# Optimization experiments

Measured on AMD Instinct MI355X. Metric: run time of the kernel, lower is better.

Reference implementation:

```python
import jax, jax.numpy as jnp
import numpy as np

B, T, C, H, N_LAYER, LAYER_ID = 4, 2048, 1024, 16, 12, 6
N = C // H
Q = 256  # T % 256 == 0 -> chunk size used by the module


def setup_inputs():
    key = jax.random.key(0)
    ks = jax.random.split(key, 9)
    r0 = LAYER_ID / (N_LAYER - 1)
    r1 = 1.0 - LAYER_ID / N_LAYER
    ddd = (jnp.arange(C, dtype=jnp.float32) / C)[None, None, :]
    h = jnp.arange(C, dtype=jnp.float32)
    s = 1.0 / np.sqrt(C)
    return {
        "x": jax.random.normal(ks[0], (B, T, C), jnp.float32),
        "time_maa_x": 1.0 - ddd ** r1,
        "time_maa_w": 1.0 - ddd ** r1,
        "time_maa_k": 1.0 - ddd ** r1,
        "time_maa_v": 1.0 - (ddd ** r1 + 0.3 * r0),
        "time_maa_r": 1.0 - ddd ** (0.5 * r1),
        "maa_w1": jax.random.uniform(ks[1], (C, 4 * 32), jnp.float32, minval=-0.01, maxval=0.01),
        "maa_w2": jax.random.uniform(ks[2], (4, 32, C), jnp.float32, minval=-0.01, maxval=0.01),
        "decay_w1": jax.random.uniform(ks[3], (C, 64), jnp.float32, minval=-0.01, maxval=0.01),
        "decay_w2": jax.random.uniform(ks[4], (64, C), jnp.float32, minval=-0.01, maxval=0.01),
        "time_decay": (-6.0 + 5.0 * (h / (C - 1)) ** (0.7 + 1.3 * r0))[None, None, :],
        "time_faaaa": (r0 * (1.0 - h / (C - 1))).reshape(1, H, 1, 1, N),
        "Wr": jax.random.normal(ks[5], (C, C), jnp.float32) * s,
        "Wk": jax.random.normal(ks[6], (C, C), jnp.float32) * s,
        "Wv": jax.random.normal(ks[7], (C, C), jnp.float32) * s,
        "Wo": jax.random.normal(ks[8], (C, C), jnp.float32) * s,
        "ln_g": jnp.ones((C,), jnp.float32),
        "ln_b": jnp.zeros((C,), jnp.float32),
    }


def _forward(x, time_maa_x, time_maa_w, time_maa_k, time_maa_v, time_maa_r,
             maa_w1, maa_w2, decay_w1, decay_w2, time_decay, time_faaaa,
             Wr, Wk, Wv, Wo, ln_g, ln_b):
    b, t, c = x.shape
    nc = t // Q
    # time_shift: zero-pad one step at front of time axis, drop last step
    xx = jnp.pad(x, ((0, 0), (1, 0), (0, 0)))[:, :-1] - x
    xxx = x + xx * time_maa_x
    m = jnp.tanh(xxx @ maa_w1).reshape(b, t, 4, -1)  # [B,T,4,32]
    m = jnp.einsum('btfd,fdc->fbtc', m, maa_w2)       # [4,B,T,C]
    mw, mk, mv, mr = m[0], m[1], m[2], m[3]
    xw = x + xx * (time_maa_w + mw)
    xk = x + xx * (time_maa_k + mk)
    xv = x + xx * (time_maa_v + mv)
    xr = x + xx * (time_maa_r + mr)
    r = (xr @ Wr).reshape(b, t, H, N).transpose(0, 2, 1, 3)  # [B,H,T,N]
    k = (xk @ Wk).reshape(b, t, H, N).transpose(0, 2, 1, 3)
    v = (xv @ Wv).reshape(b, t, H, N).transpose(0, 2, 1, 3)
    w = time_decay + jnp.tanh(xw @ decay_w1) @ decay_w2      # [B,T,C]
    w = w.reshape(b, t, H, N).transpose(0, 2, 1, 3).mean(axis=-1)  # [B,H,T]
    w_log = -jnp.exp(w)
    wc = w_log.reshape(b, H, nc, Q, 1)
    wc_cum = jnp.cumsum(wc, axis=-2)
    shifted = jnp.pad(wc_cum, ((0, 0), (0, 0), (0, 0), (1, 0), (0, 0)))[..., :-1, :]
    ws_log = wc.sum(axis=-2, keepdims=True)   # [B,H,nc,1,1]
    w_inter = jnp.exp(ws_log - wc_cum)        # [B,H,nc,Q,1]
    w_intra = jnp.exp(wc_cum - wc)            # [B,H,nc,Q,1]
    ws = jnp.exp(ws_log)                      # [B,H,nc,1,1]
    A = shifted - jnp.swapaxes(wc_cum, -1, -2)  # [B,H,nc,Q,Q]
    strict = jnp.tril(jnp.ones((Q, Q), dtype=bool), -1)
    # torch: tril() -> exp() -> tril(-1)  ==  exp on strict-lower, zero elsewhere
    w_mask = jnp.where(strict, jnp.exp(jnp.where(strict, A, 0.0)), 0.0)
    rr = r.reshape(b, H, nc, Q, N)
    kk = k.reshape(b, H, nc, Q, N)
    vv = v.reshape(b, H, nc, Q, N)
    kv = jnp.einsum('bhcqn,bhcqm->bhcnm', kk * w_inter, vv)  # [B,H,nc,N,N]

    def step(state, inp):
        ws_i, kv_i = inp
        return ws_i * state + kv_i, state  # emit state BEFORE update (as in torch loop)

    _, states = jax.lax.scan(step, jnp.zeros((b, H, N, N), x.dtype),
                             (jnp.moveaxis(ws, 2, 0), jnp.moveaxis(kv, 2, 0)))
    states = jnp.moveaxis(states, 0, 2)  # [B,H,nc,N,N]
    inter = jnp.einsum('bhcqn,bhcnm->bhcqm', rr * w_intra, states)
    scores = jnp.einsum('bhcqn,bhckn->bhcqk', rr, kk) * w_mask
    diag = jnp.sum(rr * (time_faaaa * kk), axis=-1)  # [B,H,nc,Q]
    intra = jnp.einsum('bhcqk,bhckm->bhcqm', scores, vv) + diag[..., None] * vv
    y = (inter + intra).reshape(b, H, t, N).transpose(0, 2, 1, 3).reshape(b, t, c)
    mu = y.mean(axis=-1, keepdims=True)
    var = ((y - mu) ** 2).mean(axis=-1, keepdims=True)
    y = (y - mu) / jnp.sqrt(var + 1e-5) * ln_g + ln_b  # ln_x
    return y @ Wo  # output projection (dropout p=0)


def reference(x, time_maa_x, time_maa_w, time_maa_k, time_maa_v, time_maa_r,
              maa_w1, maa_w2, decay_w1, decay_w2, time_decay, time_faaaa,
              Wr, Wk, Wv, Wo, ln_g, ln_b):
    return _forward(x, time_maa_x, time_maa_w, time_maa_k, time_maa_v, time_maa_r,
                    maa_w1, maa_w2, decay_w1, decay_w2, time_decay, time_faaaa,
                    Wr, Wk, Wv, Wo, ln_g, ln_b)
```

## Files before the change

kernel.cpp:

```cpp
#include <hip/hip_runtime.h>
#include <math.h>

#define BB 4
#define TT 2048
#define CC 1024
#define HH 16
#define NN 64
#define QQ 256
#define NCH 8
#define BT 8192

typedef unsigned short u16;
typedef __attribute__((ext_vector_type(8))) short bf16x8;
typedef __attribute__((ext_vector_type(4))) short bf16x4;
typedef __attribute__((ext_vector_type(4))) float f32x4;
typedef __attribute__((ext_vector_type(4))) u16 u16x4;

__device__ inline u16 f2b(float x) {
  union { float f; unsigned u; } v;
  v.f = x;
  unsigned r = v.u + 0x7FFFu + ((v.u >> 16) & 1u);
  return (u16)(r >> 16);
}
__device__ inline float b2f(u16 u) {
  union { unsigned u; float f; } v;
  v.u = ((unsigned)u) << 16;
  return v.f;
}
__device__ inline bf16x8 ldfrag(const u16* p) {
  bf16x4 lo = *(const bf16x4*)p;
  bf16x4 hi = *(const bf16x4*)(p + 4);
  return __builtin_shufflevector(lo, hi, 0, 1, 2, 3, 4, 5, 6, 7);
}
__device__ inline void stage_tile(const u16* __restrict__ g, size_t base,
                                  int pitch, int tid, u16* __restrict__ lds) {
#pragma unroll
  for (int it = 0; it < 2; it++) {
    int cidx = tid + it * 256;
    int r = cidx >> 3, c8 = (cidx & 7) * 8;
    bf16x8 v = *(const bf16x8*)(g + base + (size_t)r * pitch + c8);
    *(bf16x4*)(lds + r * 72 + c8) = __builtin_shufflevector(v, v, 0, 1, 2, 3);
    *(bf16x4*)(lds + r * 72 + c8 + 4) = __builtin_shufflevector(v, v, 4, 5, 6, 7);
  }
}

__global__ __launch_bounds__(256) void mix_kernel(const float* __restrict__ x,
                                                  const float* __restrict__ tmx,
                                                  u16* __restrict__ xxxb) {
  size_t e = ((size_t)blockIdx.x * 256 + threadIdx.x) * 4;
  int c = (int)(e & 1023);
  size_t row = e >> 10;
  int t = (int)(row & 2047);
  float4 xv = *(const float4*)(x + e);
  float4 pv = make_float4(0.f, 0.f, 0.f, 0.f);
  if (t > 0) pv = *(const float4*)(x + e - 1024);
  float4 d = make_float4(pv.x - xv.x, pv.y - xv.y, pv.z - xv.z, pv.w - xv.w);
  u16x4 o;
  o.x = f2b(xv.x + d.x * tmx[c + 0]);
  o.y = f2b(xv.y + d.y * tmx[c + 1]);
  o.z = f2b(xv.z + d.z * tmx[c + 2]);
  o.w = f2b(xv.w + d.w * tmx[c + 3]);
  *(u16x4*)(xxxb + e) = o;
}

__global__ __launch_bounds__(256) void cvt_wT(const float* __restrict__ W0,
                                              const float* __restrict__ W1,
                                              const float* __restrict__ W2,
                                              const float* __restrict__ W3,
                                              u16* __restrict__ O0,
                                              u16* __restrict__ O1,
                                              u16* __restrict__ O2,
                                              u16* __restrict__ O3) {
  const float* W;
  u16* O;
  switch (blockIdx.z) {
    case 0: W = W0; O = O0; break;
    case 1: W = W1; O = O1; break;
    case 2: W = W2; O = O2; break;
    default: W = W3; O = O3; break;
  }
  __shared__ float t[64][65];
  int bx = blockIdx.x * 64;
  int by = blockIdx.y * 64;
#pragma unroll
  for (int it = 0; it < 16; it++) {
    int idx = it * 256 + threadIdx.x;
    int r = idx >> 6, c = idx & 63;
    t[r][c] = W[(size_t)(by + r) * 1024 + bx + c];
  }
  __syncthreads();
#pragma unroll
  for (int it = 0; it < 16; it++) {
    int idx = it * 256 + threadIdx.x;
    int n = idx >> 6, k = idx & 63;
    O[(size_t)(bx + n) * 1024 + by + k] = f2b(t[k][n]);
  }
}

__global__ __launch_bounds__(256) void cvt3_T(const float* __restrict__ w1,
                                              const float* __restrict__ w2,
                                              const float* __restrict__ d1,
                                              u16* __restrict__ o1,
                                              u16* __restrict__ o2,
                                              u16* __restrict__ o3) {
  const float* in;
  u16* out;
  int R, C;
  switch (blockIdx.z) {
    case 0: in = w1; out = o1; R = 1024; C = 128; break;
    case 1: in = w2; out = o2; R = 128; C = 1024; break;
    default: in = d1; out = o3; R = 1024; C = 64; break;
  }
  int c0 = blockIdx.x * 64, r0 = blockIdx.y * 64;
  if (c0 >= C || r0 >= R) return;
  __shared__ float t[64][65];
#pragma unroll
  for (int it = 0; it < 16; it++) {
    int idx = it * 256 + threadIdx.x;
    int r = idx >> 6, c = idx & 63;
    t[r][c] = in[(size_t)(r0 + r) * C + c0 + c];
  }
  __syncthreads();
#pragma unroll
  for (int it = 0; it < 16; it++) {
    int idx = it * 256 + threadIdx.x;
    int c = idx >> 6, r = idx & 63;
    out[(size_t)(c0 + c) * R + r0 + r] = f2b(t[r][c]);
  }
}

__global__ __launch_bounds__(256) void gemm_maa(const u16* __restrict__ A,
                                                const u16* __restrict__ Bt,
                                                u16* __restrict__ Cb) {
  __shared__ u16 As[64 * 32];
  __shared__ u16 Bs[128 * 32];
  const int tid = threadIdx.x;
  const int lane = tid & 63;
  const int wave = tid >> 6;
  const int wc = wave * 32;
  const int fr = lane & 15;
  const int fq = lane >> 4;
  const int row0 = blockIdx.x * 64;

  f32x4 acc[4][2];
#pragma unroll
  for (int i = 0; i < 4; i++)
#pragma unroll
    for (int j = 0; j < 2; j++) acc[i][j] = (f32x4){0.f, 0.f, 0.f, 0.f};

  const int ra = tid >> 2, ca = (tid & 3) * 8;
  const int rb1 = ra + 64;

  for (int k0 = 0; k0 < 1024; k0 += 32) {
    __builtin_amdgcn_global_load_lds(
        (const __attribute__((address_space(1))) void*)(A + (size_t)(row0 + ra) * 1024 + k0 + ca),
        (__attribute__((address_space(3))) void*)(As + tid * 8), 16, 0, 0);
    __builtin_amdgcn_global_load_lds(
        (const __attribute__((address_space(1))) void*)(Bt + (size_t)ra * 1024 + k0 + ca),
        (__attribute__((address_space(3))) void*)(Bs + tid * 8), 16, 0, 0);
    __builtin_amdgcn_global_load_lds(
        (const __attribute__((address_space(1))) void*)(Bt + (size_t)rb1 * 1024 + k0 + ca),
        (__attribute__((address_space(3))) void*)(Bs + (tid + 256) * 8), 16, 0, 0);
    __syncthreads();
    bf16x8 af[4], bf[2];
#pragma unroll
    for (int i = 0; i < 4; i++)
      af[i] = *(const bf16x8*)(As + ((i * 16 + fr) * 32 + fq * 8));
#pragma unroll
    for (int j = 0; j < 2; j++)
      bf[j] = *(const bf16x8*)(Bs + ((wc + j * 16 + fr) * 32 + fq * 8));
#pragma unroll
    for (int i = 0; i < 4; i++)
#pragma unroll
      for (int j = 0; j < 2; j++)
        acc[i][j] = __builtin_amdgcn_mfma_f32_16x16x32_bf16(af[i], bf[j], acc[i][j], 0, 0, 0);
    __syncthreads();
  }
#pragma unroll
  for (int i = 0; i < 4; i++) {
    int grow = row0 + i * 16 + fq * 4;
#pragma unroll
    for (int j = 0; j < 2; j++) {
      int gcol = wc + j * 16 + fr;
#pragma unroll
      for (int r = 0; r < 4; r++)
        Cb[(size_t)(grow + r) * 128 + gcol] = f2b(tanhf(acc[i][j][r]));
    }
  }
}

#define DP_ABUF 8192
#define DP_BBUF 16384
#define DP_SBUF 24576
#define DP_SMEM_BYTES 147456

template <bool TRIPLE, bool F32OUT>
__global__ __launch_bounds__(512, 2) void gemm_dp(
    const u16* __restrict__ A0, const u16* __restrict__ A1,
    const u16* __restrict__ A2, const u16* __restrict__ B0,
    const u16* __restrict__ B1, const u16* __restrict__ B2,
    float* __restrict__ Cf, u16* __restrict__ C0, u16* __restrict__ C1,
    u16* __restrict__ C2) {
  extern __shared__ __align__(16) u16 smem[];
  const int nwg = (int)(gridDim.x * gridDim.y * gridDim.z);
  const int wg = (int)(blockIdx.x + (blockIdx.y << 2) + (blockIdx.z << 8));
  const int cpx = nwg >> 3;
  const int swz = (wg & 7) * cpx + (wg >> 3);
  const int bx = swz & 3;
  const int by = (swz >> 2) & 63;
  const int bz = swz >> 8;

  const u16* __restrict__ A;
  const u16* __restrict__ Bt;
  u16* __restrict__ Cb;
  if (TRIPLE) {
    switch (bz) {
      case 0: A = A0; Bt = B0; Cb = C0; break;
      case 1: A = A1; Bt = B1; Cb = C1; break;
      default: A = A2; Bt = B2; Cb = C2; break;
    }
  } else {
    A = A0; Bt = B0; Cb = C0;
  }

  const int tid = threadIdx.x;
  const int lane = tid & 63;
  const int wave = tid >> 6;
  const int wr = (wave >> 2) * 64;
  const int wc = (wave & 3) * 64;
  const int fr = lane & 15;
  const int fq = lane >> 4;
  const int s8 = fr & 7;
  const int row0 = by * 128;
  const int col0 = bx * 256;

  int aoff[4][2], boff[4][2];
#pragma unroll
  for (int mi = 0; mi < 4; mi++)
#pragma unroll
    for (int ks = 0; ks < 2; ks++)
      aoff[mi][ks] = (wr + mi * 16 + fr) * 64 + (((ks * 4 + fq) ^ s8) * 8);
#pragma unroll
  for (int nj = 0; nj < 4; nj++)
#pragma unroll
    for (int ks = 0; ks < 2; ks++)
      boff[nj][ks] = (wc + nj * 16 + fr) * 64 + (((ks * 4 + fq) ^ s8) * 8);

  auto stage = [&](int kt, int q) {
    const u16* __restrict__ gA = A + (size_t)row0 * 1024 + kt * 64;
    const u16* __restrict__ gB = Bt + (size_t)col0 * 1024 + kt * 64;
    u16* dA = smem + q * DP_SBUF;
    u16* dB = dA + DP_ABUF;
#pragma unroll
    for (int p = 0; p < 2; p++) {
      int pos = tid + p * 512;
      int r = pos >> 3, gch = (pos & 7) ^ (r & 7);
      __builtin_amdgcn_global_load_lds(
          (const __attribute__((address_space(1))) void*)(gA + (size_t)r * 1024 + gch * 8),
          (__attribute__((address_space(3))) void*)(dA + pos * 8), 16, 0, 0);
    }
#pragma unroll
    for (int p = 0; p < 4; p++) {
      int pos = tid + p * 512;
      int r = pos >> 3, gch = (pos & 7) ^ (r & 7);
      __builtin_amdgcn_global_load_lds(
          (const __attribute__((address_space(1))) void*)(gB + (size_t)r * 1024 + gch * 8),
          (__attribute__((address_space(3))) void*)(dB + pos * 8), 16, 0, 0);
    }
  };

  f32x4 acc[4][4];
#pragma unroll
  for (int mi = 0; mi < 4; mi++)
#pragma unroll
    for (int nj = 0; nj < 4; nj++) acc[mi][nj] = (f32x4){0.f, 0.f, 0.f, 0.f};

  auto iter_body = [&](int qc, int qs, bool dostage, int t2) {
    if (dostage) stage(t2, qs);
    const u16* sA = smem + qc * DP_SBUF;
    const u16* sB = sA + DP_ABUF;
    bf16x8 av[4][2], bv[4][2];
#pragma unroll
    for (int mi = 0; mi < 4; mi++)
#pragma unroll
      for (int ks = 0; ks < 2; ks++)
        av[mi][ks] = *(const bf16x8*)(sA + aoff[mi][ks]);
#pragma unroll
    for (int nj = 0; nj < 4; nj++)
#pragma unroll
      for (int ks = 0; ks < 2; ks++)
        bv[nj][ks] = *(const bf16x8*)(sB + boff[nj][ks]);
    __builtin_amdgcn_s_setprio(1);
#pragma unroll
    for (int ks = 0; ks < 2; ks++)
#pragma unroll
      for (int mi = 0; mi < 4; mi++)
#pragma unroll
        for (int nj = 0; nj < 4; nj++)
          acc[mi][nj] = __builtin_amdgcn_mfma_f32_16x16x32_bf16(
              av[mi][ks], bv[nj][ks], acc[mi][nj], 0, 0, 0);
    __builtin_amdgcn_s_setprio(0);
  };

  stage(0, 0);
  stage(1, 1);
  int qc = 0, qs = 2;
  for (int t = 0; t < 14; t++) {
    asm volatile("s_waitcnt vmcnt(6)" ::: "memory");
    __builtin_amdgcn_s_barrier();
    iter_body(qc, qs, true, t + 2);
    qc = (qc == 2) ? 0 : qc + 1;
    qs = (qs == 2) ? 0 : qs + 1;
  }
  asm volatile("s_waitcnt vmcnt(6)" ::: "memory");
  __builtin_amdgcn_s_barrier();
  iter_body(qc, 0, false, 0);
  qc = (qc == 2) ? 0 : qc + 1;
  asm volatile("s_waitcnt vmcnt(0)" ::: "memory");
  __builtin_amdgcn_s_barrier();
  iter_body(qc, 0, false, 0);

#pragma unroll
  for (int mi = 0; mi < 4; mi++) {
    int grow = row0 + wr + mi * 16 + fq * 4;
#pragma unroll
    for (int nj = 0; nj < 4; nj++) {
      int gcol = col0 + wc + nj * 16 + fr;
#pragma unroll
      for (int r = 0; r < 4; r++) {
        if (F32OUT)
          Cf[(size_t)(grow + r) * 1024 + gcol] = acc[mi][nj][r];
        else
          Cb[(size_t)(grow + r) * 1024 + gcol] = f2b(acc[mi][nj][r]);
      }
    }
  }
}

__global__ __launch_bounds__(256) void blend_mfma(
    const u16* __restrict__ mb, const u16* __restrict__ w2T,
    const float* __restrict__ x,
    const float* __restrict__ tmw, const float* __restrict__ tmk,
    const float* __restrict__ tmv, const float* __restrict__ tmr,
    u16* __restrict__ xwb, u16* __restrict__ xkb, u16* __restrict__ xvb,
    u16* __restrict__ xrb) {
  __shared__ u16 mS[64 * 136];
  __shared__ u16 wS[64 * 136];
  const int tid = threadIdx.x;
  const int lane = tid & 63;
  const int w = tid >> 6;
  const int fr = lane & 15;
  const int fq = lane >> 4;
  const int c0 = blockIdx.x * 64;
  const int bt0 = blockIdx.y * 64;

#pragma unroll
  for (int it = 0; it < 4; it++) {
    int idx = tid + it * 256;
    int r = idx >> 4, c8 = (idx & 15) * 8;
    bf16x8 v = *(const bf16x8*)(mb + (size_t)(bt0 + r) * 128 + c8);
    *(bf16x4*)(mS + r * 136 + c8) = __builtin_shufflevector(v, v, 0, 1, 2, 3);
    *(bf16x4*)(mS + r * 136 + c8 + 4) = __builtin_shufflevector(v, v, 4, 5, 6, 7);
    bf16x8 u = *(const bf16x8*)(w2T + (size_t)(c0 + r) * 128 + c8);
    *(bf16x4*)(wS + r * 136 + c8) = __builtin_shufflevector(u, u, 0, 1, 2, 3);
    *(bf16x4*)(wS + r * 136 + c8 + 4) = __builtin_shufflevector(u, u, 4, 5, 6, 7);
  }
  __syncthreads();

  f32x4 acc[4][4];
#pragma unroll
  for (int j = 0; j < 4; j++)
#pragma unroll
    for (int f = 0; f < 4; f++) acc[j][f] = (f32x4){0.f, 0.f, 0.f, 0.f};

#pragma unroll
  for (int f = 0; f < 4; f++) {
    bf16x8 aA = ldfrag(mS + (w * 16 + fr) * 136 + f * 32 + fq * 8);
#pragma unroll
    for (int j = 0; j < 4; j++) {
      bf16x8 bB = ldfrag(wS + (j * 16 + fr) * 136 + f * 32 + fq * 8);
      acc[j][f] = __builtin_amdgcn_mfma_f32_16x16x32_bf16(aA, bB, acc[j][f], 0, 0, 0);
    }
  }

#pragma unroll
  for (int j = 0; j < 4; j++) {
    int c = c0 + j * 16 + fr;
    float w_ = tmw[c], k_ = tmk[c], v_ = tmv[c], r_ = tmr[c];
#pragma unroll
    for (int rr = 0; rr < 4; rr++) {
      int bt = bt0 + w * 16 + fq * 4 + rr;
      size_t g = (size_t)bt * 1024 + c;
      float xv_ = x[g];
      float xp = ((bt & 2047) != 0) ? x[g - 1024] : 0.f;
      float dx = xp - xv_;
      xwb[g] = f2b(xv_ + dx * (w_ + acc[j][0][rr]));
      xkb[g] = f2b(xv_ + dx * (k_ + acc[j][1][rr]));
      xvb[g] = f2b(xv_ + dx * (v_ + acc[j][2][rr]));
      xrb[g] = f2b(xv_ + dx * (r_ + acc[j][3][rr]));
    }
  }
}

__global__ __launch_bounds__(256) void dw2r_kernel(const float* __restrict__ dw2,
                                                   const float* __restrict__ td,
                                                   float* __restrict__ dw2r,
                                                   float* __restrict__ tdr,
                                                   u16* __restrict__ dw2rbT) {
  int idx = blockIdx.x * 256 + threadIdx.x;
  if (idx < 1024) {
    int j = idx >> 4, h = idx & 15;
    float s = 0.f;
    for (int n = 0; n < 64; n++) s += dw2[(size_t)j * 1024 + h * 64 + n];
    float m = s * (1.f / 64.f);
    dw2r[j * 16 + h] = m;
    dw2rbT[h * 64 + j] = f2b(m);
  }
  if (idx < 16) {
    float s = 0.f;
    for (int n = 0; n < 64; n++) s += td[idx * 64 + n];
    tdr[idx] = s * (1.f / 64.f);
  }
}

__global__ __launch_bounds__(256) void decay_mfma(const u16* __restrict__ xwb,
                                                  const u16* __restrict__ d1T,
                                                  const u16* __restrict__ dw2rbT,
                                                  const float* __restrict__ tdr,
                                                  float* __restrict__ wlog) {
  __shared__ u16 As[64 * 32];
  __shared__ u16 Bs[64 * 32];
  __shared__ u16 h1S[64 * 72];
  __shared__ u16 dwS[16 * 72];
  const int tid = threadIdx.x;
  const int lane = tid & 63;
  const int w = tid >> 6;
  const int fr = lane & 15;
  const int fq = lane >> 4;
  const int bt0 = blockIdx.x * 64;

#pragma unroll
  for (int it = 0; it < 4; it++) {
    int idx = tid + it * 256;
    int r = idx >> 6, c = idx & 63;
    dwS[r * 72 + c] = dw2rbT[r * 64 + c];
  }

  f32x4 acc[4];
#pragma unroll
  for (int j = 0; j < 4; j++) acc[j] = (f32x4){0.f, 0.f, 0.f, 0.f};

  const int ra = tid >> 2, ca = (tid & 3) * 8;
  for (int k0 = 0; k0 < 1024; k0 += 32) {
    __builtin_amdgcn_global_load_lds(
        (const __attribute__((address_space(1))) void*)(xwb + (size_t)(bt0 + ra) * 1024 + k0 + ca),
        (__attribute__((address_space(3))) void*)(As + tid * 8), 16, 0, 0);
    __builtin_amdgcn_global_load_lds(
        (const __attribute__((address_space(1))) void*)(d1T + (size_t)ra * 1024 + k0 + ca),
        (__attribute__((address_space(3))) void*)(Bs + tid * 8), 16, 0, 0);
    __syncthreads();
    bf16x8 aA = *(const bf16x8*)(As + ((w * 16 + fr) * 32 + fq * 8));
#pragma unroll
    for (int j = 0; j < 4; j++) {
      bf16x8 bB = *(const bf16x8*)(Bs + ((j * 16 + fr) * 32 + fq * 8));
      acc[j] = __builtin_amdgcn_mfma_f32_16x16x32_bf16(aA, bB, acc[j], 0, 0, 0);
    }
    __syncthreads();
  }
#pragma unroll
  for (int j = 0; j < 4; j++)
#pragma unroll
    for (int rr = 0; rr < 4; rr++)
      h1S[(w * 16 + fq * 4 + rr) * 72 + j * 16 + fr] = f2b(tanhf(acc[j][rr]));
  __syncthreads();

  f32x4 a2 = (f32x4){0.f, 0.f, 0.f, 0.f};
#pragma unroll
  for (int ks = 0; ks < 2; ks++) {
    bf16x8 aA = ldfrag(h1S + (w * 16 + fr) * 72 + ks * 32 + fq * 8);
    bf16x8 bB = ldfrag(dwS + fr * 72 + ks * 32 + fq * 8);
    a2 = __builtin_amdgcn_mfma_f32_16x16x32_bf16(aA, bB, a2, 0, 0, 0);
  }
  float tdv = tdr[fr];
#pragma unroll
  for (int rr = 0; rr < 4; rr++) {
    int bt = bt0 + w * 16 + fq * 4 + rr;
    int b = bt >> 11, tl = bt & 2047;
    wlog[((size_t)(b * 16 + fr)) * 2048 + tl] = -__expf(tdv + a2[rr]);
  }
}

__global__ __launch_bounds__(256) void wprep_kernel(const float* __restrict__ wlog,
                                                    float* __restrict__ cum,
                                                    float* __restrict__ excl,
                                                    float* __restrict__ wsl) {
  int bid = blockIdx.x;
  int c = bid & 7, bh = bid >> 3;
  int q = threadIdx.x;
  float v = wlog[(size_t)bh * 2048 + c * 256 + q];
  __shared__ float s[256];
  s[q] = v;
  float val = v;
  for (int off = 1; off < 256; off <<= 1) {
    __syncthreads();
    float t = (q >= off) ? s[q - off] : 0.f;
    __syncthreads();
    val += t;
    s[q] = val;
  }
  __syncthreads();
  float total = s[255];
  cum[(size_t)bid * 256 + q] = val;
  excl[(size_t)bid * 256 + q] = val - v;
  if (q == 0) wsl[bid] = total;
}

__global__ __launch_bounds__(256) void kvtrans2_kernel(
    const u16* __restrict__ vb, const u16* __restrict__ kb,
    const u16* __restrict__ rb, const float* __restrict__ faaaa,
    const float* __restrict__ cum, const float* __restrict__ wsl,
    u16* __restrict__ vT, u16* __restrict__ kTw, float* __restrict__ diagG) {
  int tt = blockIdx.x;
  int bh = blockIdx.y;
  int b = bh >> 4, h = bh & 15;
  int cc = tt >> 2;
  int bidc = bh * 8 + cc;
  __shared__ float tv[64][65];
  __shared__ float tk[64][65];
  __shared__ float wfac[64];
  __shared__ float faS[64];
  const int tid = threadIdx.x;
  float wslog = wsl[bidc];
  if (tid < 64) {
    wfac[tid] = __expf(wslog - cum[(size_t)bidc * 256 + (tt & 3) * 64 + tid]);
    faS[tid] = faaaa[h * 64 + tid];
  }
  __syncthreads();
  const int m = tid & 63;
  float fam = faS[m];
#pragma unroll
  for (int it = 0; it < 16; it++) {
    int r = it * 4 + (tid >> 6);
    size_t g = ((size_t)(b * TT + tt * 64 + r)) * CC + h * 64 + m;
    float vraw = b2f(vb[g]);
    float kraw = b2f(kb[g]);
    float rraw = b2f(rb[g]);
    tv[r][m] = vraw;
    tk[r][m] = kraw;
    float s = rraw * fam * kraw;
    s += __shfl_xor(s, 1);
    s += __shfl_xor(s, 2);
    s += __shfl_xor(s, 4);
    s += __shfl_xor(s, 8);
    s += __shfl_xor(s, 16);
    s += __shfl_xor(s, 32);
    if (m == 0) diagG[(size_t)bh * 2048 + tt * 64 + r] = s;
  }
  __syncthreads();
#pragma unroll
  for (int it = 0; it < 16; it++) {
    int idx = it * 256 + tid;
    int mm = idx >> 6, tl = idx & 63;
    size_t o = ((size_t)(bh * 64 + mm)) * TT + tt * 64 + tl;
    vT[o] = f2b(tv[tl][mm]);
    kTw[o] = f2b(tk[tl][mm] * wfac[tl]);
  }
}

__global__ __launch_bounds__(256) void kv_mfma(const u16* __restrict__ kTw,
                                               const u16* __restrict__ vT,
                                               float* __restrict__ kvb) {
  int bid = blockIdx.x;
  int c = bid & 7, bh = bid >> 3;
  __shared__ u16 kS[64 * 72];
  __shared__ u16 vS[64 * 72];
  const int tid = threadIdx.x;
  const int lane = tid & 63;
  const int w = tid >> 6;
  const int fr = lane & 15;
  const int fq = lane >> 4;
  f32x4 acc[4];
#pragma unroll
  for (int j = 0; j < 4; j++) acc[j] = (f32x4){0.f, 0.f, 0.f, 0.f};
  const size_t base = (size_t)bh * 64 * TT + c * QQ;
  for (int qt = 0; qt < 4; qt++) {
    __syncthreads();
    stage_tile(kTw, base + qt * 64, TT, tid, kS);
    stage_tile(vT, base + qt * 64, TT, tid, vS);
    __syncthreads();
#pragma unroll
    for (int ks = 0; ks < 2; ks++) {
      bf16x8 aA = ldfrag(kS + (w * 16 + fr) * 72 + ks * 32 + fq * 8);
#pragma unroll
      for (int j = 0; j < 4; j++) {
        bf16x8 bB = ldfrag(vS + (j * 16 + fr) * 72 + ks * 32 + fq * 8);
        acc[j] = __builtin_amdgcn_mfma_f32_16x16x32_bf16(aA, bB, acc[j], 0, 0, 0);
      }
    }
  }
#pragma unroll
  for (int j = 0; j < 4; j++)
#pragma unroll
    for (int rr = 0; rr < 4; rr++)
      kvb[(size_t)bid * 4096 + (w * 16 + fq * 4 + rr) * 64 + j * 16 + fr] = acc[j][rr];
}

__global__ __launch_bounds__(256) void scan_kernel(const float* __restrict__ kvb,
                                                   const float* __restrict__ wsl,
                                                   float* __restrict__ st) {
  int bh = blockIdx.x >> 2;
  int sl = blockIdx.x & 3;
  int tid = threadIdx.x;
  float s[4];
#pragma unroll
  for (int i = 0; i < 4; i++) s[i] = 0.f;
  for (int c = 0; c < 8; c++) {
    int bid = bh * 8 + c;
    float w = __expf(wsl[bid]);
#pragma unroll
    for (int i = 0; i < 4; i++) {
      size_t e = (size_t)bid * 4096 + sl * 1024 + i * 256 + tid;
      st[e] = s[i];
      s[i] = w * s[i] + kvb[e];
    }
  }
}

__global__ __launch_bounds__(256) void attn_mfma(
    const u16* __restrict__ rb, const u16* __restrict__ kb,
    const u16* __restrict__ vT, const float* __restrict__ stg,
    const float* __restrict__ cum, const float* __restrict__ excl,
    const float* __restrict__ diagG, float* __restrict__ y) {
  int bid = blockIdx.x;
  int c = bid & 7, bh = bid >> 3;
  int b = bh >> 4, h = bh & 15;
  __shared__ u16 rt[64 * 72];
  __shared__ u16 kt[64 * 72];
  __shared__ u16 vt[64 * 72];
  __shared__ u16 pt[64 * 72];
  __shared__ u16 stT[64 * 72];
  __shared__ float cumS[256], exS[256], diagS[256], ekS[256];

  const int tid = threadIdx.x;
  const int lane = tid & 63;
  const int w = tid >> 6;
  const int fr = lane & 15;
  const int fq = lane >> 4;

  cumS[tid] = cum[(size_t)bid * 256 + tid];
  exS[tid] = excl[(size_t)bid * 256 + tid];
  diagS[tid] = diagG[(size_t)bh * 2048 + c * 256 + tid];
#pragma unroll
  for (int it = 0; it < 16; it++) {
    int idx = tid + it * 256;
    int n = idx >> 6, mm = idx & 63;
    stT[mm * 72 + n] = f2b(stg[(size_t)bid * 4096 + idx]);
  }
  __syncthreads();
  const float ccm = cumS[127];
  ekS[tid] = __expf(ccm - cumS[tid]);

  const size_t rowbase = ((size_t)b * TT + c * QQ) * CC + h * 64;
  const size_t vbase0 = (size_t)bh * 64 * TT + c * QQ;

  for (int qt = 0; qt < 4; qt++) {
    __syncthreads();
    stage_tile(rb, rowbase + (size_t)(qt * 64) * CC, CC, tid, rt);
    __syncthreads();

    f32x4 acc[4];
#pragma unroll
    for (int jm = 0; jm < 4; jm++) acc[jm] = (f32x4){0.f, 0.f, 0.f, 0.f};
    bf16x8 rA[2];
    rA[0] = ldfrag(rt + (w * 16 + fr) * 72 + fq * 8);
    rA[1] = ldfrag(rt + (w * 16 + fr) * 72 + 32 + fq * 8);
#pragma unroll
    for (int ks = 0; ks < 2; ks++)
#pragma unroll
      for (int jm = 0; jm < 4; jm++) {
        bf16x8 bB = ldfrag(stT + (jm * 16 + fr) * 72 + ks * 32 + fq * 8);
        acc[jm] = __builtin_amdgcn_mfma_f32_16x16x32_bf16(rA[ks], bB, acc[jm], 0, 0, 0);
      }
    int ql0 = w * 16 + fq * 4;
    float er[4], eqc[4];
#pragma unroll
    for (int rr = 0; rr < 4; rr++) {
      float ex = exS[qt * 64 + ql0 + rr];
      er[rr] = __expf(ex);
      eqc[rr] = __expf(ex - ccm);
    }
#pragma unroll
    for (int jm = 0; jm < 4; jm++)
#pragma unroll
      for (int rr = 0; rr < 4; rr++) acc[jm][rr] *= er[rr];

    for (int kti = 0; kti <= qt; kti++) {
      __syncthreads();
      stage_tile(kb, rowbase + (size_t)(kti * 64) * CC, CC, tid, kt);
      stage_tile(vT, vbase0 + (size_t)(kti * 64), TT, tid, vt);
      __syncthreads();

      f32x4 sacc[4];
#pragma unroll
      for (int jj = 0; jj < 4; jj++) sacc[jj] = (f32x4){0.f, 0.f, 0.f, 0.f};
#pragma unroll
      for (int ks = 0; ks < 2; ks++)
#pragma unroll
        for (int jj = 0; jj < 4; jj++) {
          bf16x8 bB = ldfrag(kt + (jj * 16 + fr) * 72 + ks * 32 + fq * 8);
          sacc[jj] = __builtin_amdgcn_mfma_f32_16x16x32_bf16(rA[ks], bB, sacc[jj], 0, 0, 0);
        }
#pragma unroll
      for (int jj = 0; jj < 4; jj++) {
        int kcol = kti * 64 + jj * 16 + fr;
        float ek = ekS[kcol];
#pragma unroll
        for (int rr = 0; rr < 4; rr++) {
          int qrow = qt * 64 + ql0 + rr;
          float vsc;
          if (kcol < qrow)
            vsc = sacc[jj][rr] * eqc[rr] * ek;
          else if (kcol == qrow)
            vsc = diagS[qrow];
          else
            vsc = 0.f;
          pt[(ql0 + rr) * 72 + jj * 16 + fr] = f2b(vsc);
        }
      }
      __syncthreads();
#pragma unroll
      for (int ks = 0; ks < 2; ks++) {
        bf16x8 pA = ldfrag(pt + (w * 16 + fr) * 72 + ks * 32 + fq * 8);
#pragma unroll
        for (int jm = 0; jm < 4; jm++) {
          bf16x8 vB = ldfrag(vt + (jm * 16 + fr) * 72 + ks * 32 + fq * 8);
          acc[jm] = __builtin_amdgcn_mfma_f32_16x16x32_bf16(pA, vB, acc[jm], 0, 0, 0);
        }
      }
    }
    int qg0 = qt * 64 + w * 16 + fq * 4;
#pragma unroll
    for (int jm = 0; jm < 4; jm++)
#pragma unroll
      for (int rr = 0; rr < 4; rr++)
        y[rowbase + (size_t)(qg0 + rr) * CC + jm * 16 + fr] = acc[jm][rr];
  }
}

__global__ __launch_bounds__(256) void ln_kernel(const float* __restrict__ y,
                                                 const float* __restrict__ g,
                                                 const float* __restrict__ bta,
                                                 u16* __restrict__ out) {
  __shared__ float red[8];
  int bt = blockIdx.x;
  int tid = threadIdx.x;
  float v[4];
  float s = 0.f;
#pragma unroll
  for (int i = 0; i < 4; i++) {
    v[i] = y[(size_t)bt * 1024 + i * 256 + tid];
    s += v[i];
  }
#pragma unroll
  for (int off = 32; off > 0; off >>= 1) s += __shfl_down(s, off);
  if ((tid & 63) == 0) red[tid >> 6] = s;
  __syncthreads();
  if (tid == 0) red[4] = red[0] + red[1] + red[2] + red[3];
  __syncthreads();
  float mu = red[4] * (1.f / 1024.f);
  float s2 = 0.f;
#pragma unroll
  for (int i = 0; i < 4; i++) {
    float d = v[i] - mu;
    s2 += d * d;
  }
#pragma unroll
  for (int off = 32; off > 0; off >>= 1) s2 += __shfl_down(s2, off);
  __syncthreads();
  if ((tid & 63) == 0) red[tid >> 6] = s2;
  __syncthreads();
  if (tid == 0) red[5] = red[0] + red[1] + red[2] + red[3];
  __syncthreads();
  float var = red[5] * (1.f / 1024.f);
  float rstd = rsqrtf(var + 1e-5f);
#pragma unroll
  for (int i = 0; i < 4; i++) {
    int c = i * 256 + tid;
    out[(size_t)bt * 1024 + c] = f2b((v[i] - mu) * rstd * g[c] + bta[c]);
  }
}

extern "C" void kernel_launch(void* const* d_in, const int* in_sizes, int n_in,
                              void* d_out, int out_size, void* d_ws,
                              size_t ws_size, hipStream_t stream) {
  const float* x = (const float*)d_in[0];
  const float* tmx = (const float*)d_in[1];
  const float* tmw = (const float*)d_in[2];
  const float* tmk = (const float*)d_in[3];
  const float* tmv = (const float*)d_in[4];
  const float* tmr = (const float*)d_in[5];
  const float* maa_w1 = (const float*)d_in[6];
  const float* maa_w2 = (const float*)d_in[7];
  const float* decay_w1 = (const float*)d_in[8];
  const float* decay_w2 = (const float*)d_in[9];
  const float* time_decay = (const float*)d_in[10];
  const float* faaaa = (const float*)d_in[11];
  const float* Wr = (const float*)d_in[12];
  const float* Wk = (const float*)d_in[13];
  const float* Wv = (const float*)d_in[14];
  const float* Wo = (const float*)d_in[15];
  const float* lng = (const float*)d_in[16];
  const float* lnb = (const float*)d_in[17];
  float* out = (float*)d_out;
  float* ws = (float*)d_ws;

  const size_t S = (size_t)BT * CC;

  float* y_ = ws;
  float* dw2r = ws + S;
  float* tdr = dw2r + 1024;
  float* wlog = tdr + 1024;
  float* cum = wlog + 131072;
  float* excl = cum + 131072;
  float* wsl = excl + 131072;
  float* diagG = wsl + 1024;
  float* kvb = diagG + 131072;
  float* stb = kvb + (size_t)512 * 4096;
  float* fend = stb + (size_t)512 * 4096;
  u16* xxxb = (u16*)fend;
  u16* mb = xxxb + S;
  u16* xkb = mb + (size_t)BT * 128;
  u16* xvb = xkb + S;
  u16* xrb = xvb + S;
  u16* xwb = xrb + S;
  u16* rb16 = xwb + S;
  u16* kb16 = rb16 + S;
  u16* Vb = kb16 + S;
  u16* Wrt = Vb + S;
  u16* Wkt = Wrt + (size_t)1024 * 1024;
  u16* Wvt = Wkt + (size_t)1024 * 1024;
  u16* Wot = Wvt + (size_t)1024 * 1024;
  u16* w1T = Wot + (size_t)1024 * 1024;
  u16* w2T = w1T + (size_t)128 * 1024;
  u16* d1T = w2T + (size_t)1024 * 128;
  u16* dw2rbT = d1T + (size_t)64 * 1024;
  u16* vT = xxxb;
  u16* kTw = xrb;
  u16* ylnb = xkb;

  static bool attr_done = false;
  if (!attr_done) {
    hipFuncSetAttribute((const void*)gemm_dp<true, false>,
                        hipFuncAttributeMaxDynamicSharedMemorySize, DP_SMEM_BYTES);
    hipFuncSetAttribute((const void*)gemm_dp<false, true>,
                        hipFuncAttributeMaxDynamicSharedMemorySize, DP_SMEM_BYTES);
    attr_done = true;
  }

  cvt_wT<<<dim3(16, 16, 4), 256, 0, stream>>>(Wr, Wk, Wv, Wo, Wrt, Wkt, Wvt, Wot);
  cvt3_T<<<dim3(16, 16, 3), 256, 0, stream>>>(maa_w1, maa_w2, decay_w1, w1T,
                                              w2T, d1T);
  dw2r_kernel<<<4, 256, 0, stream>>>(decay_w2, time_decay, dw2r, tdr, dw2rbT);
  mix_kernel<<<8192, 256, 0, stream>>>(x, tmx, xxxb);
  gemm_maa<<<128, 256, 0, stream>>>(xxxb, w1T, mb);
  blend_mfma<<<dim3(16, 128), 256, 0, stream>>>(mb, w2T, x, tmw, tmk, tmv, tmr,
                                                xwb, xkb, xvb, xrb);
  decay_mfma<<<128, 256, 0, stream>>>(xwb, d1T, dw2rbT, tdr, wlog);
  wprep_kernel<<<512, 256, 0, stream>>>(wlog, cum, excl, wsl);
  gemm_dp<true, false><<<dim3(4, 64, 3), 512, DP_SMEM_BYTES, stream>>>(
      xrb, xkb, xvb, Wrt, Wkt, Wvt, nullptr, rb16, kb16, Vb);
  kvtrans2_kernel<<<dim3(32, 64), 256, 0, stream>>>(Vb, kb16, rb16, faaaa, cum,
                                                    wsl, vT, kTw, diagG);
  kv_mfma<<<512, 256, 0, stream>>>(kTw, vT, kvb);
  scan_kernel<<<256, 256, 0, stream>>>(kvb, wsl, stb);
  attn_mfma<<<512, 256, 0, stream>>>(rb16, kb16, vT, stb, cum, excl, diagG, y_);
  ln_kernel<<<BT, 256, 0, stream>>>(y_, lng, lnb, ylnb);
  gemm_dp<false, true><<<dim3(4, 64, 1), 512, DP_SMEM_BYTES, stream>>>(
      ylnb, nullptr, nullptr, Wot, nullptr, nullptr, out, nullptr, nullptr,
      nullptr);
}
```

Before: 365.0 us.

## Fuse transpose into kv state GEMM, merge dw2r prep, split gemm_maa columns

```diff
diff --git a/kernel.cpp b/kernel.cpp
--- a/kernel.cpp
+++ b/kernel.cpp
@@ -102,7 +102,30 @@
                                               const float* __restrict__ d1,
                                               u16* __restrict__ o1,
                                               u16* __restrict__ o2,
-                                              u16* __restrict__ o3) {
+                                              u16* __restrict__ o3,
+                                              const float* __restrict__ dw2,
+                                              const float* __restrict__ td,
+                                              float* __restrict__ dw2r,
+                                              float* __restrict__ tdr,
+                                              u16* __restrict__ dw2rbT) {
+  if (blockIdx.z == 3) {
+    if (blockIdx.y != 0 || blockIdx.x >= 4) return;
+    int idx = blockIdx.x * 256 + threadIdx.x;
+    if (idx < 1024) {
+      int j = idx >> 4, h = idx & 15;
+      float s = 0.f;
+      for (int n = 0; n < 64; n++) s += dw2[(size_t)j * 1024 + h * 64 + n];
+      float m = s * (1.f / 64.f);
+      dw2r[j * 16 + h] = m;
+      dw2rbT[h * 64 + j] = f2b(m);
+    }
+    if (idx < 16) {
+      float s = 0.f;
+      for (int n = 0; n < 64; n++) s += td[idx * 64 + n];
+      tdr[idx] = s * (1.f / 64.f);
+    }
+    return;
+  }
   const float* in;
   u16* out;
   int R, C;
@@ -133,59 +156,44 @@
                                                 const u16* __restrict__ Bt,
                                                 u16* __restrict__ Cb) {
   __shared__ u16 As[64 * 32];
-  __shared__ u16 Bs[128 * 32];
+  __shared__ u16 Bs[64 * 32];
   const int tid = threadIdx.x;
   const int lane = tid & 63;
   const int wave = tid >> 6;
-  const int wc = wave * 32;
+  const int wc = wave * 16;
   const int fr = lane & 15;
   const int fq = lane >> 4;
-  const int row0 = blockIdx.x * 64;
-
-  f32x4 acc[4][2];
-#pragma unroll
-  for (int i = 0; i < 4; i++)
-#pragma unroll
-    for (int j = 0; j < 2; j++) acc[i][j] = (f32x4){0.f, 0.f, 0.f, 0.f};
+  const int row0 = blockIdx.y * 64;
+  const int col0 = blockIdx.x * 64;
+
+  f32x4 acc[4];
+#pragma unroll
+  for (int i = 0; i < 4; i++) acc[i] = (f32x4){0.f, 0.f, 0.f, 0.f};
 
   const int ra = tid >> 2, ca = (tid & 3) * 8;
-  const int rb1 = ra + 64;
 
   for (int k0 = 0; k0 < 1024; k0 += 32) {
     __builtin_amdgcn_global_load_lds(
         (const __attribute__((address_space(1))) void*)(A + (size_t)(row0 + ra) * 1024 + k0 + ca),
         (__attribute__((address_space(3))) void*)(As + tid * 8), 16, 0, 0);
     __builtin_amdgcn_global_load_lds(
-        (const __attribute__((address_space(1))) void*)(Bt + (size_t)ra * 1024 + k0 + ca),
+        (const __attribute__((address_space(1))) void*)(Bt + (size_t)(col0 + ra) * 1024 + k0 + ca),
         (__attribute__((address_space(3))) void*)(Bs + tid * 8), 16, 0, 0);
-    __builtin_amdgcn_global_load_lds(
-        (const __attribute__((address_space(1))) void*)(Bt + (size_t)rb1 * 1024 + k0 + ca),
-        (__attribute__((address_space(3))) void*)(Bs + (tid + 256) * 8), 16, 0, 0);
-    __syncthreads();
-    bf16x8 af[4], bf[2];
-#pragma unroll
-    for (int i = 0; i < 4; i++)
-      af[i] = *(const bf16x8*)(As + ((i * 16 + fr) * 32 + fq * 8));
-#pragma unroll
-    for (int j = 0; j < 2; j++)
-      bf[j] = *(const bf16x8*)(Bs + ((wc + j * 16 + fr) * 32 + fq * 8));
-#pragma unroll
-    for (int i = 0; i < 4; i++)
-#pragma unroll
-      for (int j = 0; j < 2; j++)
-        acc[i][j] = __builtin_amdgcn_mfma_f32_16x16x32_bf16(af[i], bf[j], acc[i][j], 0, 0, 0);
+    __syncthreads();
+    bf16x8 bf = *(const bf16x8*)(Bs + ((wc + fr) * 32 + fq * 8));
+#pragma unroll
+    for (int i = 0; i < 4; i++) {
+      bf16x8 af = *(const bf16x8*)(As + ((i * 16 + fr) * 32 + fq * 8));
+      acc[i] = __builtin_amdgcn_mfma_f32_16x16x32_bf16(af, bf, acc[i], 0, 0, 0);
+    }
     __syncthreads();
   }
 #pragma unroll
   for (int i = 0; i < 4; i++) {
     int grow = row0 + i * 16 + fq * 4;
 #pragma unroll
-    for (int j = 0; j < 2; j++) {
-      int gcol = wc + j * 16 + fr;
-#pragma unroll
-      for (int r = 0; r < 4; r++)
-        Cb[(size_t)(grow + r) * 128 + gcol] = f2b(tanhf(acc[i][j][r]));
-    }
+    for (int r = 0; r < 4; r++)
+      Cb[(size_t)(grow + r) * 128 + col0 + wc + fr] = f2b(tanhf(acc[i][r]));
   }
 }
 
@@ -402,27 +410,6 @@
   }
 }
 
-__global__ __launch_bounds__(256) void dw2r_kernel(const float* __restrict__ dw2,
-                                                   const float* __restrict__ td,
-                                                   float* __restrict__ dw2r,
-                                                   float* __restrict__ tdr,
-                                                   u16* __restrict__ dw2rbT) {
-  int idx = blockIdx.x * 256 + threadIdx.x;
-  if (idx < 1024) {
-    int j = idx >> 4, h = idx & 15;
-    float s = 0.f;
-    for (int n = 0; n < 64; n++) s += dw2[(size_t)j * 1024 + h * 64 + n];
-    float m = s * (1.f / 64.f);
-    dw2r[j * 16 + h] = m;
-    dw2rbT[h * 64 + j] = f2b(m);
-  }
-  if (idx < 16) {
-    float s = 0.f;
-    for (int n = 0; n < 64; n++) s += td[idx * 64 + n];
-    tdr[idx] = s * (1.f / 64.f);
-  }
-}
-
 __global__ __launch_bounds__(256) void decay_mfma(const u16* __restrict__ xwb,
                                                   const u16* __restrict__ d1T,
                                                   const u16* __restrict__ dw2rbT,
@@ -515,85 +502,76 @@
   if (q == 0) wsl[bid] = total;
 }
 
-__global__ __launch_bounds__(256) void kvtrans2_kernel(
+__global__ __launch_bounds__(256) void kvfuse_kernel(
     const u16* __restrict__ vb, const u16* __restrict__ kb,
     const u16* __restrict__ rb, const float* __restrict__ faaaa,
     const float* __restrict__ cum, const float* __restrict__ wsl,
-    u16* __restrict__ vT, u16* __restrict__ kTw, float* __restrict__ diagG) {
-  int tt = blockIdx.x;
-  int bh = blockIdx.y;
+    u16* __restrict__ vT, float* __restrict__ diagG, float* __restrict__ kvb) {
+  int bid = blockIdx.x;
+  int c = bid & 7, bh = bid >> 3;
   int b = bh >> 4, h = bh & 15;
-  int cc = tt >> 2;
-  int bidc = bh * 8 + cc;
   __shared__ float tv[64][65];
   __shared__ float tk[64][65];
-  __shared__ float wfac[64];
+  __shared__ u16 kSb[64 * 72];
+  __shared__ u16 vSb[64 * 72];
+  __shared__ float wfacS[256];
   __shared__ float faS[64];
-  const int tid = threadIdx.x;
-  float wslog = wsl[bidc];
-  if (tid < 64) {
-    wfac[tid] = __expf(wslog - cum[(size_t)bidc * 256 + (tt & 3) * 64 + tid]);
-    faS[tid] = faaaa[h * 64 + tid];
-  }
-  __syncthreads();
-  const int m = tid & 63;
-  float fam = faS[m];
-#pragma unroll
-  for (int it = 0; it < 16; it++) {
-    int r = it * 4 + (tid >> 6);
-    size_t g = ((size_t)(b * TT + tt * 64 + r)) * CC + h * 64 + m;
-    float vraw = b2f(vb[g]);
-    float kraw = b2f(kb[g]);
-    float rraw = b2f(rb[g]);
-    tv[r][m] = vraw;
-    tk[r][m] = kraw;
-    float s = rraw * fam * kraw;
-    s += __shfl_xor(s, 1);
-    s += __shfl_xor(s, 2);
-    s += __shfl_xor(s, 4);
-    s += __shfl_xor(s, 8);
-    s += __shfl_xor(s, 16);
-    s += __shfl_xor(s, 32);
-    if (m == 0) diagG[(size_t)bh * 2048 + tt * 64 + r] = s;
-  }
-  __syncthreads();
-#pragma unroll
-  for (int it = 0; it < 16; it++) {
-    int idx = it * 256 + tid;
-    int mm = idx >> 6, tl = idx & 63;
-    size_t o = ((size_t)(bh * 64 + mm)) * TT + tt * 64 + tl;
-    vT[o] = f2b(tv[tl][mm]);
-    kTw[o] = f2b(tk[tl][mm] * wfac[tl]);
-  }
-}
-
-__global__ __launch_bounds__(256) void kv_mfma(const u16* __restrict__ kTw,
-                                               const u16* __restrict__ vT,
-                                               float* __restrict__ kvb) {
-  int bid = blockIdx.x;
-  int c = bid & 7, bh = bid >> 3;
-  __shared__ u16 kS[64 * 72];
-  __shared__ u16 vS[64 * 72];
   const int tid = threadIdx.x;
   const int lane = tid & 63;
   const int w = tid >> 6;
   const int fr = lane & 15;
   const int fq = lane >> 4;
+  const int m = lane;
+
+  float wslog = wsl[bid];
+  wfacS[tid] = __expf(wslog - cum[(size_t)bid * 256 + tid]);
+  if (tid < 64) faS[tid] = faaaa[h * 64 + tid];
+
   f32x4 acc[4];
 #pragma unroll
   for (int j = 0; j < 4; j++) acc[j] = (f32x4){0.f, 0.f, 0.f, 0.f};
-  const size_t base = (size_t)bh * 64 * TT + c * QQ;
+
   for (int qt = 0; qt < 4; qt++) {
     __syncthreads();
-    stage_tile(kTw, base + qt * 64, TT, tid, kS);
-    stage_tile(vT, base + qt * 64, TT, tid, vS);
+    float fam = faS[m];
+    int t0 = c * QQ + qt * 64;
+#pragma unroll
+    for (int it = 0; it < 16; it++) {
+      int r = it * 4 + w;
+      size_t g = ((size_t)(b * TT + t0 + r)) * CC + h * 64 + m;
+      float vraw = b2f(vb[g]);
+      float kraw = b2f(kb[g]);
+      float rraw = b2f(rb[g]);
+      tv[r][m] = vraw;
+      tk[r][m] = kraw;
+      float s = rraw * fam * kraw;
+      s += __shfl_xor(s, 1);
+      s += __shfl_xor(s, 2);
+      s += __shfl_xor(s, 4);
+      s += __shfl_xor(s, 8);
+      s += __shfl_xor(s, 16);
+      s += __shfl_xor(s, 32);
+      if (m == 0) diagG[(size_t)bh * 2048 + t0 + r] = s;
+    }
+    __syncthreads();
+#pragma unroll
+    for (int it = 0; it < 16; it++) {
+      int idx = it * 256 + tid;
+      int mm = idx >> 6, tl = idx & 63;
+      float vv = tv[tl][mm];
+      float kk = tk[tl][mm] * wfacS[qt * 64 + tl];
+      u16 vbv = f2b(vv);
+      vT[((size_t)(bh * 64 + mm)) * TT + t0 + tl] = vbv;
+      vSb[mm * 72 + tl] = vbv;
+      kSb[mm * 72 + tl] = f2b(kk);
+    }
     __syncthreads();
 #pragma unroll
     for (int ks = 0; ks < 2; ks++) {
-      bf16x8 aA = ldfrag(kS + (w * 16 + fr) * 72 + ks * 32 + fq * 8);
+      bf16x8 aA = ldfrag(kSb + (w * 16 + fr) * 72 + ks * 32 + fq * 8);
 #pragma unroll
       for (int j = 0; j < 4; j++) {
-        bf16x8 bB = ldfrag(vS + (j * 16 + fr) * 72 + ks * 32 + fq * 8);
+        bf16x8 bB = ldfrag(vSb + (j * 16 + fr) * 72 + ks * 32 + fq * 8);
         acc[j] = __builtin_amdgcn_mfma_f32_16x16x32_bf16(aA, bB, acc[j], 0, 0, 0);
       }
     }
@@ -845,7 +823,6 @@
   u16* d1T = w2T + (size_t)1024 * 128;
   u16* dw2rbT = d1T + (size_t)64 * 1024;
   u16* vT = xxxb;
-  u16* kTw = xrb;
   u16* ylnb = xkb;
 
   static bool attr_done = false;
@@ -858,20 +835,19 @@
   }
 
   cvt_wT<<<dim3(16, 16, 4), 256, 0, stream>>>(Wr, Wk, Wv, Wo, Wrt, Wkt, Wvt, Wot);
-  cvt3_T<<<dim3(16, 16, 3), 256, 0, stream>>>(maa_w1, maa_w2, decay_w1, w1T,
-                                              w2T, d1T);
-  dw2r_kernel<<<4, 256, 0, stream>>>(decay_w2, time_decay, dw2r, tdr, dw2rbT);
+  cvt3_T<<<dim3(16, 16, 4), 256, 0, stream>>>(maa_w1, maa_w2, decay_w1, w1T,
+                                              w2T, d1T, decay_w2, time_decay,
+                                              dw2r, tdr, dw2rbT);
   mix_kernel<<<8192, 256, 0, stream>>>(x, tmx, xxxb);
-  gemm_maa<<<128, 256, 0, stream>>>(xxxb, w1T, mb);
+  gemm_maa<<<dim3(2, 128), 256, 0, stream>>>(xxxb, w1T, mb);
   blend_mfma<<<dim3(16, 128), 256, 0, stream>>>(mb, w2T, x, tmw, tmk, tmv, tmr,
                                                 xwb, xkb, xvb, xrb);
   decay_mfma<<<128, 256, 0, stream>>>(xwb, d1T, dw2rbT, tdr, wlog);
   wprep_kernel<<<512, 256, 0, stream>>>(wlog, cum, excl, wsl);
   gemm_dp<true, false><<<dim3(4, 64, 3), 512, DP_SMEM_BYTES, stream>>>(
       xrb, xkb, xvb, Wrt, Wkt, Wvt, nullptr, rb16, kb16, Vb);
-  kvtrans2_kernel<<<dim3(32, 64), 256, 0, stream>>>(Vb, kb16, rb16, faaaa, cum,
-                                                    wsl, vT, kTw, diagG);
-  kv_mfma<<<512, 256, 0, stream>>>(kTw, vT, kvb);
+  kvfuse_kernel<<<512, 256, 0, stream>>>(Vb, kb16, rb16, faaaa, cum, wsl, vT,
+                                         diagG, kvb);
   scan_kernel<<<256, 256, 0, stream>>>(kvb, wsl, stb);
   attn_mfma<<<512, 256, 0, stream>>>(rb16, kb16, vT, stb, cum, excl, diagG, y_);
   ln_kernel<<<BT, 256, 0, stream>>>(y_, lng, lnb, ylnb);
```

New measurement: 361.0 us. No clear change (-1.1%).
